# Kernel tuning notes

Hardware: AMD Instinct MI355X
Metric: run time of the kernel (lower is better)

Reference implementation:

```python
import jax, jax.numpy as jnp
import numpy as np

D = 1024
H = 16
HD = D // H
EPS = 1e-9


def setup_inputs() -> dict:
    key = jax.random.key(0)
    ks = jax.random.split(key, 16)
    B, Lq, Lk = 8, 512, 1024
    s = 0.02
    return {
        "q": jax.random.normal(ks[0], (B, Lq, D), jnp.float32),
        "q_mask": jnp.ones((B, Lq), jnp.bool_),
        "kv": jax.random.normal(ks[1], (B, Lk, D), jnp.float32),
        "kv_mask": jnp.ones((B, Lk), jnp.bool_),
        # MultiheadAttention packed in-proj + out-proj
        "in_proj_w": jax.random.normal(ks[2], (3 * D, D), jnp.float32) * s,
        "in_proj_b": jnp.zeros((3 * D,), jnp.float32),
        "out_w": jax.random.normal(ks[3], (D, D), jnp.float32) * s,
        "out_b": jnp.zeros((D,), jnp.float32),
        # shared LayerNorm
        "ln_g": jnp.ones((D,), jnp.float32),
        "ln_b": jnp.zeros((D,), jnp.float32),
        # FFN
        "w1": jax.random.normal(ks[4], (4 * D, D), jnp.float32) * s,
        "b1": jnp.zeros((4 * D,), jnp.float32),
        "w2": jax.random.normal(ks[5], (D, 4 * D), jnp.float32) * s,
        "b2": jnp.zeros((D,), jnp.float32),
        # gate MLP
        "gw1": jax.random.normal(ks[6], (D, 2 * D), jnp.float32) * s,
        "gb1": jnp.zeros((D,), jnp.float32),
        "gw2": jax.random.normal(ks[7], (1, D), jnp.float32) * s,
        "gb2": jnp.zeros((1,), jnp.float32),
    }


def _layer_norm(x, g, b, eps=1e-5):
    mu = x.mean(-1, keepdims=True)
    var = ((x - mu) ** 2).mean(-1, keepdims=True)
    return (x - mu) * jax.lax.rsqrt(var + eps) * g + b


def reference(q, q_mask, kv, kv_mask, in_proj_w, in_proj_b, out_w, out_b,
              ln_g, ln_b, w1, b1, w2, b2, gw1, gb1, gw2, gb2):
    B, Lq, _ = q.shape
    Lk = kv.shape[1]
    # packed projections (torch Linear convention: x @ W.T + b)
    qp = (q @ in_proj_w[:D].T + in_proj_b[:D]).reshape(B, Lq, H, HD)
    kp = (kv @ in_proj_w[D:2 * D].T + in_proj_b[D:2 * D]).reshape(B, Lk, H, HD)
    vp = (kv @ in_proj_w[2 * D:].T + in_proj_b[2 * D:]).reshape(B, Lk, H, HD)
    scores = jnp.einsum('bqhd,bkhd->bhqk', qp, kp) / np.sqrt(HD)  # (B,H,Lq,Lk)
    scores = jnp.where(kv_mask[:, None, None, :], scores, -1e30)
    attn = jax.nn.softmax(scores, axis=-1)
    ctx = jnp.einsum('bhqk,bkhd->bqhd', attn, vp).reshape(B, Lq, D)
    attn_out = ctx @ out_w.T + out_b
    # entropy over keys, normalized by log(Lk), averaged over heads
    p = jnp.clip(attn, EPS)
    ent = -(p * jnp.log(p)).sum(-1) / jnp.log(jnp.float32(Lk))  # (B,H,Lq)
    ent = ent.mean(axis=1)[..., None]  # (B,Lq,1)
    conf = jnp.clip(1.0 - ent, 0.0, 1.0)
    # gate MLP on [q, attn_out]
    h = jax.nn.gelu(jnp.concatenate([q, attn_out], -1) @ gw1.T + gb1, approximate=False)
    g = jax.nn.sigmoid(h @ gw2.T + gb2) * conf
    q2 = _layer_norm(q + attn_out * g, ln_g, ln_b)
    ffn = jax.nn.gelu(q2 @ w1.T + b1, approximate=False) @ w2.T + b2
    q2 = _layer_norm(q2 + ffn, ln_g, ln_b)
    return q2, ent
```

## Files before the change

kernel.cpp:

```cpp
#include <hip/hip_runtime.h>
#include <cstdint>
#include <cstddef>

typedef __bf16 bf16;
typedef __bf16 bf16x8 __attribute__((ext_vector_type(8)));
typedef __bf16 bf16x4 __attribute__((ext_vector_type(4)));
typedef float  f32x4  __attribute__((ext_vector_type(4)));

#define GLOAD_LDS16(g, l) __builtin_amdgcn_global_load_lds( \
    (const __attribute__((address_space(1))) unsigned int*)(g), \
    (__attribute__((address_space(3))) unsigned int*)(l), 16, 0, 0)

static constexpr int D_  = 1024;
static constexpr int H_  = 16;
static constexpr int HD_ = 64;
static constexpr int B_  = 8;
static constexpr int LQ_ = 512;
static constexpr int LK_ = 1024;
static constexpr int MQ_ = B_ * LQ_;
static constexpr float LOG2E_ = 1.4426950408889634f;
static constexpr float INV_LN_LK_ = 0.14426950408889634f;
static constexpr float CSHIFT_ = 8.0f;

__device__ __forceinline__ float gelu_f(float v) {
    return 0.5f * v * (1.0f + erff(v * 0.70710678118654752f));
}

__global__ __launch_bounds__(256)
void cast_all_k(const float* __restrict__ ipw, const float* __restrict__ outw,
                const float* __restrict__ w1,  const float* __restrict__ w2,
                const float* __restrict__ gw1, const float* __restrict__ q,
                const float* __restrict__ kv,
                bf16* __restrict__ ipw_b, bf16* __restrict__ outw_b,
                bf16* __restrict__ w1_b,  bf16* __restrict__ w2_b,
                bf16* __restrict__ gw1_b, bf16* __restrict__ x_b,
                bf16* __restrict__ kv_b) {
    const int b = blockIdx.x, t = threadIdx.x;
    const float* src; bf16* dst; long e;
    if (b < 1536)       { src = ipw;  dst = ipw_b;  e = (long)b * 2048; }
    else if (b < 2048)  { src = outw; dst = outw_b; e = (long)(b - 1536) * 2048; }
    else if (b < 4096)  { src = w1;   dst = w1_b;   e = (long)(b - 2048) * 2048; }
    else if (b < 6144)  { src = w2;   dst = w2_b;   e = (long)(b - 4096) * 2048; }
    else if (b < 7168)  { src = gw1;  dst = gw1_b;  e = (long)(b - 6144) * 2048; }
    else if (b < 11264) { src = kv;   dst = kv_b;   e = (long)(b - 7168) * 2048; }
    else {
        long e2 = (long)(b - 11264) * 2048 + t * 8;
        float4 a = *(const float4*)(q + e2);
        float4 c = *(const float4*)(q + e2 + 4);
        bf16x8 o;
        o[0]=(bf16)a.x; o[1]=(bf16)a.y; o[2]=(bf16)a.z; o[3]=(bf16)a.w;
        o[4]=(bf16)c.x; o[5]=(bf16)c.y; o[6]=(bf16)c.z; o[7]=(bf16)c.w;
        long row = e2 >> 10, col = e2 & 1023;
        *(bf16x8*)(x_b + row * 2048 + col) = o;
        return;
    }
    e += t * 8;
    float4 a = *(const float4*)(src + e);
    float4 c = *(const float4*)(src + e + 4);
    bf16x8 o;
    o[0]=(bf16)a.x; o[1]=(bf16)a.y; o[2]=(bf16)a.z; o[3]=(bf16)a.w;
    o[4]=(bf16)c.x; o[5]=(bf16)c.y; o[6]=(bf16)c.z; o[7]=(bf16)c.w;
    *(bf16x8*)(dst + e) = o;
}

template<int SPLITK>
__device__ __forceinline__
void gemmP_body(const bf16* __restrict__ A, int lda,
                const bf16* __restrict__ W, int ldw,
                const float* __restrict__ bias,
                bf16* __restrict__ Cb, int ldcb,
                float* __restrict__ Cf0, float* __restrict__ Cf1, int ldcf,
                int K, int aoff, int woff) {
    __shared__ __attribute__((aligned(16))) bf16 LDSp[3 * 8192];
    const int gx = gridDim.x, gy = gridDim.y;
    const int nwg = gx * gy * gridDim.z;
    const int flat = blockIdx.x + gx * (blockIdx.y + gy * blockIdx.z);
    const int swz = (flat & 7) * (nwg >> 3) + (flat >> 3);
    int rem = swz, z = 0;
    if (SPLITK) { z = swz / (gx * gy); rem = swz - z * (gx * gy); }
    const int by = rem / gx, bx = rem - by * gx;
    if (SPLITK) { A += (size_t)z * aoff; W += (size_t)z * woff; }
    float* Cf = (SPLITK && z) ? Cf1 : Cf0;

    const int t = threadIdx.x;
    const int w = t >> 6, l = t & 63, l15 = l & 15, lg = l >> 4;
    const int row0 = by * 128, col0 = bx * 128;
    const int wr = (w >> 1) * 64, wc = (w & 1) * 64;

    const int sr = t >> 2;
    const int sc = ((t & 3) ^ ((sr >> 1) & 3)) << 3;
    const bf16* pA0 = A + (size_t)(row0 + sr) * lda + sc;
    const bf16* pA1 = A + (size_t)(row0 + 64 + sr) * lda + sc;
    const bf16* pW0 = W + (size_t)(col0 + sr) * ldw + sc;
    const bf16* pW1 = W + (size_t)(col0 + 64 + sr) * ldw + sc;
    const int lo0 = w * 512, lo1 = 2048 + w * 512;

    auto STAGE = [&](int kt, int slot) {
        bf16* base = (bf16*)LDSp + slot * 8192;
        const int kc = kt * 32;
        GLOAD_LDS16(pA0 + kc, base + lo0);
        GLOAD_LDS16(pA1 + kc, base + lo1);
        GLOAD_LDS16(pW0 + kc, base + 4096 + lo0);
        GLOAD_LDS16(pW1 + kc, base + 4096 + lo1);
    };

    f32x4 acc[4][4];
#pragma unroll
    for (int m = 0; m < 4; ++m)
#pragma unroll
        for (int n = 0; n < 4; ++n) acc[m][n] = f32x4{0.f, 0.f, 0.f, 0.f};

    const int nk = K >> 5;
    STAGE(0, 0); STAGE(1, 1);
    asm volatile("s_waitcnt vmcnt(4)" ::: "memory");
    __builtin_amdgcn_s_barrier();

    int s0 = 0, s1 = 1, s2 = 2;
    const int kcol = (lg ^ ((l15 >> 1) & 3)) << 3;
    for (int kt = 0; kt < nk; ++kt) {
        const bf16* bufA = (const bf16*)LDSp + s0 * 8192;
        const bf16* bufB = bufA + 4096;
        bf16x8 af[4], bf4[4];
#pragma unroll
        for (int m = 0; m < 4; ++m)
            af[m] = *(const bf16x8*)&bufA[(wr + m * 16 + l15) * 32 + kcol];
#pragma unroll
        for (int n = 0; n < 4; ++n)
            bf4[n] = *(const bf16x8*)&bufB[(wc + n * 16 + l15) * 32 + kcol];
        if (kt + 2 < nk) STAGE(kt + 2, s2);
        __builtin_amdgcn_s_setprio(1);
#pragma unroll
        for (int m = 0; m < 4; ++m)
#pragma unroll
            for (int n = 0; n < 4; ++n)
                acc[m][n] = __builtin_amdgcn_mfma_f32_16x16x32_bf16(af[m], bf4[n], acc[m][n], 0, 0, 0);
        __builtin_amdgcn_s_setprio(0);
        asm volatile("s_waitcnt lgkmcnt(0)" ::: "memory");
        __builtin_amdgcn_sched_barrier(0);
        if (kt + 2 < nk) {
            asm volatile("s_waitcnt vmcnt(4)" ::: "memory");
        } else {
            asm volatile("s_waitcnt vmcnt(0)" ::: "memory");
        }
        __builtin_amdgcn_s_barrier();
        const int tmp = s0; s0 = s1; s1 = s2; s2 = tmp;
    }

    if (!SPLITK) {
        float bvn[4];
#pragma unroll
        for (int n = 0; n < 4; ++n) bvn[n] = bias[col0 + wc + n * 16 + l15];
        const int erow = l >> 2, ec = (l & 3) * 16;
#pragma unroll
        for (int m = 0; m < 4; ++m) {
            bf16* ep = (bf16*)LDSp + ((m & 1) * 4 + w) * 1152;
#pragma unroll
            for (int n = 0; n < 4; ++n)
#pragma unroll
                for (int r = 0; r < 4; ++r)
                    ep[(lg * 4 + r) * 72 + n * 16 + l15] = (bf16)(acc[m][n][r] + bvn[n]);
            asm volatile("s_waitcnt lgkmcnt(0)" ::: "memory");
            __builtin_amdgcn_sched_barrier(0);
            bf16x8 v8a = *(const bf16x8*)&ep[erow * 72 + ec];
            bf16x8 v8b = *(const bf16x8*)&ep[erow * 72 + ec + 8];
            const int grow = row0 + wr + m * 16 + erow;
            bf16* dst = Cb + (size_t)grow * ldcb + col0 + wc + ec;
            *(bf16x8*)dst = v8a;
            *(bf16x8*)(dst + 8) = v8b;
        }
    } else {
#pragma unroll
        for (int n = 0; n < 4; ++n) {
            int gcol = col0 + wc + n * 16 + l15;
#pragma unroll
            for (int m = 0; m < 4; ++m) {
                int grow = row0 + wr + m * 16 + lg * 4;
#pragma unroll
                for (int r = 0; r < 4; ++r)
                    Cf[(size_t)(grow + r) * ldcf + gcol] = acc[m][n][r];
            }
        }
    }
}

__global__ __launch_bounds__(256, 2)
void gemmP_qproj_k(const bf16* A, const bf16* W, const float* bias, bf16* Cb) {
    gemmP_body<0>(A, 2048, W, 1024, bias, Cb, 1024, nullptr, nullptr, 0, 1024, 0, 0);
}
__global__ __launch_bounds__(256, 2)
void gemmP_outproj_k(const bf16* A, const bf16* W, const float* bias, bf16* Cb) {
    gemmP_body<0>(A, 1024, W, 1024, bias, Cb, 2048, nullptr, nullptr, 0, 1024, 0, 0);
}
__global__ __launch_bounds__(256, 2)
void gemmP_gate2_k(const bf16* A, const bf16* W, float* C0, float* C1) {
    gemmP_body<1>(A, 2048, W, 2048, nullptr, nullptr, 0, C0, C1, 1024, 1024, 1024, 1024);
}
__global__ __launch_bounds__(256, 2)
void gemmP_ffn2_k(const bf16* A, const bf16* W, float* C0, float* C1) {
    gemmP_body<1>(A, 4096, W, 4096, nullptr, nullptr, 0, C0, C1, 1024, 2048, 2048, 2048);
}

template<int ACT>
__device__ __forceinline__
void gemm128x256_body(const bf16* __restrict__ A, int lda,
                      const bf16* __restrict__ W, int ldw,
                      const float* __restrict__ bias,
                      bf16* __restrict__ Cb, int ldcb, int K) {
    __shared__ __attribute__((aligned(16))) bf16 LDSb[2][12288];
    const int gx = gridDim.x;
    const int nwg = gx * gridDim.y;
    const int flat = blockIdx.x + gx * blockIdx.y;
    const int swz = (flat & 7) * (nwg >> 3) + (flat >> 3);
    const int by = swz / gx, bx = swz - by * gx;
    const int t = threadIdx.x;
    const int w = t >> 6, l = t & 63, l15 = l & 15, lg = l >> 4;
    const int wrr = w >> 2, wc = w & 3;
    const int row0 = by * 128, col0 = bx * 256;

    const int trow = t >> 2;
    const int scol = ((t & 3) ^ ((trow >> 1) & 3)) << 3;
    const bf16* pA  = A + (size_t)(row0 + trow) * lda + scol;
    const bf16* pB0 = W + (size_t)(col0 + trow) * ldw + scol;
    const bf16* pB1 = W + (size_t)(col0 + 128 + trow) * ldw + scol;
    const int ldsoA  = w * 512;
    const int ldsoB0 = 4096 + w * 512;
    const int ldsoB1 = 8192 + w * 512;

    f32x4 acc[4][4];
#pragma unroll
    for (int m = 0; m < 4; ++m)
#pragma unroll
        for (int n = 0; n < 4; ++n) acc[m][n] = f32x4{0.f, 0.f, 0.f, 0.f};

    const int nk = K >> 5;
    GLOAD_LDS16(pA,  (bf16*)LDSb[0] + ldsoA);
    GLOAD_LDS16(pB0, (bf16*)LDSb[0] + ldsoB0);
    GLOAD_LDS16(pB1, (bf16*)LDSb[0] + ldsoB1);

    for (int kt = 0; kt < nk; ++kt) {
        const int cur = kt & 1;
        if (kt + 1 < nk) {
            const int kc = (kt + 1) * 32;
            bf16* d = (bf16*)LDSb[cur ^ 1];
            GLOAD_LDS16(pA + kc,  d + ldsoA);
            GLOAD_LDS16(pB0 + kc, d + ldsoB0);
            GLOAD_LDS16(pB1 + kc, d + ldsoB1);
            asm volatile("s_waitcnt vmcnt(3)" ::: "memory");
        } else {
            asm volatile("s_waitcnt vmcnt(0)" ::: "memory");
        }
        __builtin_amdgcn_s_barrier();
        const bf16* bufA = (const bf16*)LDSb[cur];
        const bf16* bufB = bufA + 4096;
        const int kcol = (lg ^ ((l15 >> 1) & 3)) << 3;
        bf16x8 bf4[4];
#pragma unroll
        for (int n = 0; n < 4; ++n)
            bf4[n] = *(const bf16x8*)&bufB[(wc * 64 + n * 16 + l15) * 32 + kcol];
#pragma unroll
        for (int m = 0; m < 4; ++m) {
            bf16x8 afm = *(const bf16x8*)&bufA[(wrr * 64 + m * 16 + l15) * 32 + kcol];
#pragma unroll
            for (int n = 0; n < 4; ++n)
                acc[m][n] = __builtin_amdgcn_mfma_f32_16x16x32_bf16(afm, bf4[n], acc[m][n], 0, 0, 0);
        }
        asm volatile("s_waitcnt lgkmcnt(0)" ::: "memory");
        __builtin_amdgcn_sched_barrier(0);
        __builtin_amdgcn_s_barrier();
    }

    float bvn[4];
#pragma unroll
    for (int n = 0; n < 4; ++n) bvn[n] = bias[col0 + wc * 64 + n * 16 + l15];
    const int erow = l >> 2, ec = (l & 3) * 16;
#pragma unroll
    for (int m = 0; m < 4; ++m) {
        bf16* ep = (bf16*)LDSb + ((m & 1) * 8 + w) * 1152;
#pragma unroll
        for (int n = 0; n < 4; ++n)
#pragma unroll
            for (int r = 0; r < 4; ++r) {
                float v = acc[m][n][r] + bvn[n];
                if (ACT) v = gelu_f(v);
                ep[(lg * 4 + r) * 72 + n * 16 + l15] = (bf16)v;
            }
        asm volatile("s_waitcnt lgkmcnt(0)" ::: "memory");
        __builtin_amdgcn_sched_barrier(0);
        bf16x8 v8a = *(const bf16x8*)&ep[erow * 72 + ec];
        bf16x8 v8b = *(const bf16x8*)&ep[erow * 72 + ec + 8];
        const int grow = row0 + wrr * 64 + m * 16 + erow;
        bf16* dst = Cb + (size_t)grow * ldcb + col0 + wc * 64 + ec;
        *(bf16x8*)dst = v8a;
        *(bf16x8*)(dst + 8) = v8b;
    }
}

__global__ __launch_bounds__(512, 4)
void gemmA_kvproj_k(const bf16* A, const bf16* W, const float* bias, bf16* Cb) {
    gemm128x256_body<0>(A, 1024, W, 1024, bias, Cb, 2048, 1024);
}
__global__ __launch_bounds__(512, 4)
void gemmA_ffn1_k(const bf16* A, const bf16* W, const float* bias, bf16* Cb) {
    gemm128x256_body<1>(A, 1024, W, 1024, bias, Cb, 4096, 1024);
}

__device__ __forceinline__ float red16sum(float v) {
    v += __shfl_xor(v, 1, 64);
    v += __shfl_xor(v, 2, 64);
    v += __shfl_xor(v, 4, 64);
    v += __shfl_xor(v, 8, 64);
    return v;
}

__global__ __launch_bounds__(256)
void attn_k(const bf16* __restrict__ Qp, const bf16* __restrict__ KVp,
            bf16* __restrict__ ctx, float* __restrict__ entm) {
    __shared__ __attribute__((aligned(16))) bf16 Ks[64 * 72];
    __shared__ __attribute__((aligned(16))) bf16 Vts[64 * 72];
    __shared__ __attribute__((aligned(16))) bf16 Ps[4][16 * 72];
    const int t = threadIdx.x, w = t >> 6, l = t & 63;
    const int l15 = l & 15, lg = l >> 4;
    const int h = blockIdx.x, b = blockIdx.y, qt = blockIdx.z;
    const int qrow0 = b * LQ_ + qt * 64 + w * 16;

    bf16x8 aq[2];
#pragma unroll
    for (int kk = 0; kk < 2; ++kk)
        aq[kk] = *(const bf16x8*)(Qp + (size_t)(qrow0 + l15) * D_ + h * HD_ + kk * 32 + lg * 8);

    f32x4 o[4];
    float Zp[4], S1p[4];
#pragma unroll
    for (int n = 0; n < 4; ++n) o[n] = f32x4{0.f, 0.f, 0.f, 0.f};
#pragma unroll
    for (int r = 0; r < 4; ++r) { Zp[r] = 0.f; S1p[r] = 0.f; }

    const float K1 = 0.125f * LOG2E_;
    const float K0 = -CSHIFT_ * LOG2E_;

    for (int c = 0; c < LK_ / 64; ++c) {
        __syncthreads();
        const int kbase = b * LK_ + c * 64;
#pragma unroll
        for (int i = 0; i < 2; ++i) {
            int f = i * 256 + t;
            int key = f >> 3, seg = f & 7;
            const bf16* kvrow = KVp + (size_t)(kbase + key) * 2048 + h * HD_ + seg * 8;
            bf16x8 k8 = *(const bf16x8*)kvrow;
            bf16x8 v8 = *(const bf16x8*)(kvrow + 1024);
            *(bf16x8*)&Ks[key * 72 + seg * 8] = k8;
            int vcol = key ^ (seg << 3);
#pragma unroll
            for (int j = 0; j < 8; ++j) Vts[(seg * 8 + j) * 72 + vcol] = v8[j];
        }
        __syncthreads();

        f32x4 s[4];
#pragma unroll
        for (int n = 0; n < 4; ++n) {
            s[n] = f32x4{0.f, 0.f, 0.f, 0.f};
#pragma unroll
            for (int kk = 0; kk < 2; ++kk) {
                bf16x8 bk = *(const bf16x8*)&Ks[(n * 16 + l15) * 72 + kk * 32 + lg * 8];
                s[n] = __builtin_amdgcn_mfma_f32_16x16x32_bf16(aq[kk], bk, s[n], 0, 0, 0);
            }
        }

        float p[4][4];
#pragma unroll
        for (int r = 0; r < 4; ++r) {
#pragma unroll
            for (int n = 0; n < 4; ++n) {
                float sv = s[n][r];
                float pv = exp2f(fmaf(sv, K1, K0));
                p[n][r] = pv;
                Zp[r] += pv;
                S1p[r] = fmaf(pv, sv, S1p[r]);
            }
        }

#pragma unroll
        for (int r = 0; r < 4; ++r)
#pragma unroll
            for (int n = 0; n < 4; ++n)
                Ps[w][(lg * 4 + r) * 72 + ((n ^ lg) << 4) + l15] = (bf16)p[n][r];

        bf16x8 ap[2];
#pragma unroll
        for (int kk = 0; kk < 2; ++kk)
            ap[kk] = *(const bf16x8*)&Ps[w][l15 * 72 + ((kk * 32 + lg * 8) ^ (((l15 >> 2) & 3) << 4))];
#pragma unroll
        for (int n = 0; n < 4; ++n) {
            const int segd = (n * 2 + (l15 >> 3)) & 7;
#pragma unroll
            for (int kk = 0; kk < 2; ++kk) {
                bf16x8 bv = *(const bf16x8*)&Vts[(n * 16 + l15) * 72 + (((kk * 4 + lg) ^ segd) << 3)];
                o[n] = __builtin_amdgcn_mfma_f32_16x16x32_bf16(ap[kk], bv, o[n], 0, 0, 0);
            }
        }
    }

#pragma unroll
    for (int r = 0; r < 4; ++r) {
        float Zr = red16sum(Zp[r]);
        float S1r = red16sum(S1p[r]) * 0.125f;
        float inv = 1.0f / Zr;
        int grow = qrow0 + lg * 4 + r;
#pragma unroll
        for (int n = 0; n < 4; ++n)
            ctx[(size_t)grow * D_ + h * HD_ + n * 16 + l15] = (bf16)(o[n][r] * inv);
        if (l15 == 0) {
            float ent = (CSHIFT_ + logf(Zr) - S1r * inv) * INV_LN_LK_ * (1.0f / 16.0f);
            atomicAdd(&entm[grow], ent);
        }
    }
}

__device__ __forceinline__ float blk_sum(float v, float* sb) {
#pragma unroll
    for (int m = 1; m < 64; m <<= 1) v += __shfl_xor(v, m, 64);
    int w = threadIdx.x >> 6;
    __syncthreads();
    if ((threadIdx.x & 63) == 0) sb[w] = v;
    __syncthreads();
    return sb[0] + sb[1] + sb[2] + sb[3];
}
__device__ __forceinline__ float2 blk_sum2(float2 v, float* sb) {
#pragma unroll
    for (int m = 1; m < 64; m <<= 1) {
        v.x += __shfl_xor(v.x, m, 64);
        v.y += __shfl_xor(v.y, m, 64);
    }
    int w = threadIdx.x >> 6;
    __syncthreads();
    if ((threadIdx.x & 63) == 0) { sb[w * 2] = v.x; sb[w * 2 + 1] = v.y; }
    __syncthreads();
    return make_float2(sb[0] + sb[2] + sb[4] + sb[6], sb[1] + sb[3] + sb[5] + sb[7]);
}

__global__ __launch_bounds__(256)
void gate_ln1_k(const float* __restrict__ qin, const bf16* __restrict__ xb,
                const float* __restrict__ gp0, const float* __restrict__ gp1,
                const float* __restrict__ gb1, const float* __restrict__ gw2,
                const float* __restrict__ gb2, const float* __restrict__ entm,
                const float* __restrict__ lng, const float* __restrict__ lnb,
                float* __restrict__ q2f, bf16* __restrict__ q2b) {
    __shared__ float sb[8];
    const int row = blockIdx.x, t = threadIdx.x, c0 = t * 4;
    float4 p0 = *(const float4*)(gp0 + (size_t)row * D_ + c0);
    float4 p1 = *(const float4*)(gp1 + (size_t)row * D_ + c0);
    float4 hb = *(const float4*)(gb1 + c0);
    float h0 = gelu_f(p0.x + p1.x + hb.x);
    float h1 = gelu_f(p0.y + p1.y + hb.y);
    float h2 = gelu_f(p0.z + p1.z + hb.z);
    float h3 = gelu_f(p0.w + p1.w + hb.w);
    float4 g4 = *(const float4*)(gw2 + c0);
    float dot = h0 * g4.x + h1 * g4.y + h2 * g4.z + h3 * g4.w;
    dot = blk_sum(dot, sb);
    float g = 1.0f / (1.0f + expf(-(dot + gb2[0])));
    float conf = fminf(fmaxf(1.0f - entm[row], 0.0f), 1.0f);
    g *= conf;
    float4 qv = *(const float4*)(qin + (size_t)row * D_ + c0);
    bf16x4 a4 = *(const bf16x4*)(xb + (size_t)row * 2048 + 1024 + c0);
    float y[4] = { qv.x + (float)a4[0] * g, qv.y + (float)a4[1] * g,
                   qv.z + (float)a4[2] * g, qv.w + (float)a4[3] * g };
    float2 ss = blk_sum2(make_float2(y[0] + y[1] + y[2] + y[3],
                                     y[0]*y[0] + y[1]*y[1] + y[2]*y[2] + y[3]*y[3]), sb);
    float mu = ss.x * (1.0f / D_);
    float var = ss.y * (1.0f / D_) - mu * mu;
    float rs = rsqrtf(var + 1e-5f);
    float4 gg = *(const float4*)(lng + c0);
    float4 bb = *(const float4*)(lnb + c0);
    float o0 = (y[0] - mu) * rs * gg.x + bb.x;
    float o1 = (y[1] - mu) * rs * gg.y + bb.y;
    float o2 = (y[2] - mu) * rs * gg.z + bb.z;
    float o3 = (y[3] - mu) * rs * gg.w + bb.w;
    *(float4*)(q2f + (size_t)row * D_ + c0) = make_float4(o0, o1, o2, o3);
    bf16x4 ob; ob[0] = (bf16)o0; ob[1] = (bf16)o1; ob[2] = (bf16)o2; ob[3] = (bf16)o3;
    *(bf16x4*)(q2b + (size_t)row * D_ + c0) = ob;
}

__global__ __launch_bounds__(256)
void ln2_k(const float* __restrict__ q2f, const float* __restrict__ fp0,
           const float* __restrict__ fp1, const float* __restrict__ b2,
           const float* __restrict__ lng, const float* __restrict__ lnb,
           float* __restrict__ outp) {
    __shared__ float sb[8];
    const int row = blockIdx.x, t = threadIdx.x, c0 = t * 4;
    float4 a = *(const float4*)(q2f + (size_t)row * D_ + c0);
    float4 f0 = *(const float4*)(fp0 + (size_t)row * D_ + c0);
    float4 f1 = *(const float4*)(fp1 + (size_t)row * D_ + c0);
    float4 bv = *(const float4*)(b2 + c0);
    float y[4] = { a.x + f0.x + f1.x + bv.x, a.y + f0.y + f1.y + bv.y,
                   a.z + f0.z + f1.z + bv.z, a.w + f0.w + f1.w + bv.w };
    float2 ss = blk_sum2(make_float2(y[0] + y[1] + y[2] + y[3],
                                     y[0]*y[0] + y[1]*y[1] + y[2]*y[2] + y[3]*y[3]), sb);
    float mu = ss.x * (1.0f / D_);
    float var = ss.y * (1.0f / D_) - mu * mu;
    float rs = rsqrtf(var + 1e-5f);
    float4 gg = *(const float4*)(lng + c0);
    float4 bb = *(const float4*)(lnb + c0);
    *(float4*)(outp + (size_t)row * D_ + c0) = make_float4(
        (y[0] - mu) * rs * gg.x + bb.x, (y[1] - mu) * rs * gg.y + bb.y,
        (y[2] - mu) * rs * gg.z + bb.z, (y[3] - mu) * rs * gg.w + bb.w);
}

extern "C" void kernel_launch(void* const* d_in, const int* in_sizes, int n_in,
                              void* d_out, int out_size, void* d_ws, size_t ws_size,
                              hipStream_t stream) {
    (void)in_sizes; (void)n_in; (void)out_size; (void)ws_size;
    const float* q    = (const float*)d_in[0];
    const float* kv   = (const float*)d_in[2];
    const float* ipw  = (const float*)d_in[4];
    const float* ipb  = (const float*)d_in[5];
    const float* outw = (const float*)d_in[6];
    const float* outb = (const float*)d_in[7];
    const float* lng  = (const float*)d_in[8];
    const float* lnb  = (const float*)d_in[9];
    const float* w1   = (const float*)d_in[10];
    const float* b1   = (const float*)d_in[11];
    const float* w2   = (const float*)d_in[12];
    const float* b2   = (const float*)d_in[13];
    const float* gw1  = (const float*)d_in[14];
    const float* gb1  = (const float*)d_in[15];
    const float* gw2  = (const float*)d_in[16];
    const float* gb2  = (const float*)d_in[17];

    char* ws = (char*)d_ws;
    const size_t MB = 1u << 20;
    bf16*  ipw_b  = (bf16*)(ws + 0);
    bf16*  outw_b = (bf16*)(ws + 6 * MB);
    bf16*  w1_b   = (bf16*)(ws + 8 * MB);
    bf16*  w2_b   = (bf16*)(ws + 16 * MB);
    bf16*  gw1_b  = (bf16*)(ws + 24 * MB);
    bf16*  x_b    = (bf16*)(ws + 28 * MB);
    bf16*  kv_b   = (bf16*)(ws + 44 * MB);
    bf16*  Qp     = (bf16*)(ws + 60 * MB);
    bf16*  KVp    = (bf16*)(ws + 68 * MB);
    bf16*  ctx    = (bf16*)(ws + 100 * MB);
    float* gp0    = (float*)(ws + 44 * MB);
    float* gp1    = (float*)(ws + 60 * MB);
    float* q2f    = (float*)(ws + 76 * MB);
    bf16*  q2b    = (bf16*)(ws + 100 * MB);
    bf16*  h1     = (bf16*)(ws + 44 * MB);
    float* fp0    = (float*)(ws + 28 * MB);
    float* fp1    = (float*)(ws + 0);

    float* out  = (float*)d_out;
    float* entm = out + (size_t)MQ_ * D_;

    (void)hipMemsetAsync(entm, 0, (size_t)MQ_ * sizeof(float), stream);

    cast_all_k<<<13312, 256, 0, stream>>>(ipw, outw, w1, w2, gw1, q, kv,
                                          ipw_b, outw_b, w1_b, w2_b, gw1_b, x_b, kv_b);

    gemmP_qproj_k<<<dim3(8, 32), 256, 0, stream>>>(x_b, ipw_b, ipb, Qp);
    gemmA_kvproj_k<<<dim3(8, 64), 512, 0, stream>>>(kv_b, ipw_b + 1024 * 1024, ipb + 1024, KVp);
    attn_k<<<dim3(H_, B_, LQ_ / 64), 256, 0, stream>>>(Qp, KVp, ctx, entm);
    gemmP_outproj_k<<<dim3(8, 32), 256, 0, stream>>>(ctx, outw_b, outb, x_b + 1024);
    gemmP_gate2_k<<<dim3(8, 32, 2), 256, 0, stream>>>(x_b, gw1_b, gp0, gp1);
    gate_ln1_k<<<MQ_, 256, 0, stream>>>(q, x_b, gp0, gp1, gb1, gw2, gb2, entm, lng, lnb, q2f, q2b);
    gemmA_ffn1_k<<<dim3(16, 32), 512, 0, stream>>>(q2b, w1_b, b1, h1);
    gemmP_ffn2_k<<<dim3(8, 32, 2), 256, 0, stream>>>(h1, w2_b, fp0, fp1);
    ln2_k<<<MQ_, 256, 0, stream>>>(q2f, fp0, fp1, b2, lng, lnb, out);
}
```

Before: 295.1 us.

## Produce transposed V from projection GEMM and double-buffer K/V via direct LDS loads

Splits the fused KV projection into a K projection and a V projection computed as W_v·kv^T, so V is written already transposed (head-dim major) with a per-row bias. The attention kernel then stages K and V tiles with global_load_lds into double-buffered, XOR-swizzled LDS and prefetches the next chunk while computing the current one. This removes the scalar in-LDS transpose of V and the register round-trip through LDS. In exchange there is an extra GEMM launch, and the transposed-output GEMM writes long rows with a strided layout.

```diff
diff --git a/kernel.cpp b/kernel.cpp
--- a/kernel.cpp
+++ b/kernel.cpp
@@ -18,6 +18,7 @@
 static constexpr int LQ_ = 512;
 static constexpr int LK_ = 1024;
 static constexpr int MQ_ = B_ * LQ_;
+static constexpr int MK_ = B_ * LK_;
 static constexpr float LOG2E_ = 1.4426950408889634f;
 static constexpr float INV_LN_LK_ = 0.14426950408889634f;
 static constexpr float CSHIFT_ = 8.0f;
@@ -200,7 +201,7 @@
     gemmP_body<1>(A, 4096, W, 4096, nullptr, nullptr, 0, C0, C1, 1024, 2048, 2048, 2048);
 }
 
-template<int ACT>
+template<int ACT, int ROWBIAS>
 __device__ __forceinline__
 void gemm128x256_body(const bf16* __restrict__ A, int lda,
                       const bf16* __restrict__ W, int ldw,
@@ -269,18 +270,26 @@
         __builtin_amdgcn_s_barrier();
     }
 
+    const int erow = l >> 2, ec = (l & 3) * 16;
     float bvn[4];
-#pragma unroll
-    for (int n = 0; n < 4; ++n) bvn[n] = bias[col0 + wc * 64 + n * 16 + l15];
-    const int erow = l >> 2, ec = (l & 3) * 16;
+    if (!ROWBIAS) {
+#pragma unroll
+        for (int n = 0; n < 4; ++n) bvn[n] = bias[col0 + wc * 64 + n * 16 + l15];
+    }
 #pragma unroll
     for (int m = 0; m < 4; ++m) {
+        float bvr[4];
+        if (ROWBIAS) {
+#pragma unroll
+            for (int r = 0; r < 4; ++r)
+                bvr[r] = bias[row0 + wrr * 64 + m * 16 + lg * 4 + r];
+        }
         bf16* ep = (bf16*)LDSb + ((m & 1) * 8 + w) * 1152;
 #pragma unroll
         for (int n = 0; n < 4; ++n)
 #pragma unroll
             for (int r = 0; r < 4; ++r) {
-                float v = acc[m][n][r] + bvn[n];
+                float v = acc[m][n][r] + (ROWBIAS ? bvr[r] : bvn[n]);
                 if (ACT) v = gelu_f(v);
                 ep[(lg * 4 + r) * 72 + n * 16 + l15] = (bf16)v;
             }
@@ -296,12 +305,16 @@
 }
 
 __global__ __launch_bounds__(512, 4)
-void gemmA_kvproj_k(const bf16* A, const bf16* W, const float* bias, bf16* Cb) {
-    gemm128x256_body<0>(A, 1024, W, 1024, bias, Cb, 2048, 1024);
+void gemmA_kproj_k(const bf16* A, const bf16* W, const float* bias, bf16* Cb) {
+    gemm128x256_body<0, 0>(A, 1024, W, 1024, bias, Cb, 1024, 1024);
+}
+__global__ __launch_bounds__(512, 4)
+void gemmA_vprojT_k(const bf16* A, const bf16* W, const float* bias, bf16* Cb) {
+    gemm128x256_body<0, 1>(A, 1024, W, 1024, bias, Cb, 8192, 1024);
 }
 __global__ __launch_bounds__(512, 4)
 void gemmA_ffn1_k(const bf16* A, const bf16* W, const float* bias, bf16* Cb) {
-    gemm128x256_body<1>(A, 1024, W, 1024, bias, Cb, 4096, 1024);
+    gemm128x256_body<1, 0>(A, 1024, W, 1024, bias, Cb, 4096, 1024);
 }
 
 __device__ __forceinline__ float red16sum(float v) {
@@ -313,10 +326,11 @@
 }
 
 __global__ __launch_bounds__(256)
-void attn_k(const bf16* __restrict__ Qp, const bf16* __restrict__ KVp,
-            bf16* __restrict__ ctx, float* __restrict__ entm) {
-    __shared__ __attribute__((aligned(16))) bf16 Ks[64 * 72];
-    __shared__ __attribute__((aligned(16))) bf16 Vts[64 * 72];
+void attn_k(const bf16* __restrict__ Qp, const bf16* __restrict__ Kp,
+            const bf16* __restrict__ Vt, bf16* __restrict__ ctx,
+            float* __restrict__ entm) {
+    __shared__ __attribute__((aligned(16))) bf16 Ks[2][64 * 64];
+    __shared__ __attribute__((aligned(16))) bf16 Vs[2][64 * 64];
     __shared__ __attribute__((aligned(16))) bf16 Ps[4][16 * 72];
     const int t = threadIdx.x, w = t >> 6, l = t & 63;
     const int l15 = l & 15, lg = l >> 4;
@@ -328,6 +342,22 @@
     for (int kk = 0; kk < 2; ++kk)
         aq[kk] = *(const bf16x8*)(Qp + (size_t)(qrow0 + l15) * D_ + h * HD_ + kk * 32 + lg * 8);
 
+    const int r0 = t >> 3, r1 = 32 + (t >> 3), j = t & 7;
+    const bf16* pK0 = Kp + (size_t)(b * LK_ + r0) * 1024 + h * HD_ + ((j ^ (r0 & 7)) << 3);
+    const bf16* pK1 = Kp + (size_t)(b * LK_ + r1) * 1024 + h * HD_ + ((j ^ (r1 & 7)) << 3);
+    const bf16* pV0 = Vt + (size_t)(h * HD_ + r0) * (size_t)MK_ + b * LK_ + ((j ^ (r0 & 7)) << 3);
+    const bf16* pV1 = Vt + (size_t)(h * HD_ + r1) * (size_t)MK_ + b * LK_ + ((j ^ (r1 & 7)) << 3);
+    const int ldsoL = w * 512, ldsoH = 2048 + w * 512;
+
+    auto STAGE = [&](int c, int buf) {
+        const size_t kadv = (size_t)c * 64 * 1024;
+        const size_t vadv = (size_t)c * 64;
+        GLOAD_LDS16(pK0 + kadv, (bf16*)Ks[buf] + ldsoL);
+        GLOAD_LDS16(pK1 + kadv, (bf16*)Ks[buf] + ldsoH);
+        GLOAD_LDS16(pV0 + vadv, (bf16*)Vs[buf] + ldsoL);
+        GLOAD_LDS16(pV1 + vadv, (bf16*)Vs[buf] + ldsoH);
+    };
+
     f32x4 o[4];
     float Zp[4], S1p[4];
 #pragma unroll
@@ -337,23 +367,15 @@
 
     const float K1 = 0.125f * LOG2E_;
     const float K0 = -CSHIFT_ * LOG2E_;
+    const int swk = l15 & 7;
+
+    STAGE(0, 0);
+    asm volatile("s_waitcnt vmcnt(0)" ::: "memory");
+    __builtin_amdgcn_s_barrier();
 
     for (int c = 0; c < LK_ / 64; ++c) {
-        __syncthreads();
-        const int kbase = b * LK_ + c * 64;
-#pragma unroll
-        for (int i = 0; i < 2; ++i) {
-            int f = i * 256 + t;
-            int key = f >> 3, seg = f & 7;
-            const bf16* kvrow = KVp + (size_t)(kbase + key) * 2048 + h * HD_ + seg * 8;
-            bf16x8 k8 = *(const bf16x8*)kvrow;
-            bf16x8 v8 = *(const bf16x8*)(kvrow + 1024);
-            *(bf16x8*)&Ks[key * 72 + seg * 8] = k8;
-            int vcol = key ^ (seg << 3);
-#pragma unroll
-            for (int j = 0; j < 8; ++j) Vts[(seg * 8 + j) * 72 + vcol] = v8[j];
-        }
-        __syncthreads();
+        const int buf = c & 1;
+        if (c + 1 < LK_ / 64) STAGE(c + 1, buf ^ 1);
 
         f32x4 s[4];
 #pragma unroll
@@ -361,7 +383,7 @@
             s[n] = f32x4{0.f, 0.f, 0.f, 0.f};
 #pragma unroll
             for (int kk = 0; kk < 2; ++kk) {
-                bf16x8 bk = *(const bf16x8*)&Ks[(n * 16 + l15) * 72 + kk * 32 + lg * 8];
+                bf16x8 bk = *(const bf16x8*)&Ks[buf][(n * 16 + l15) * 64 + ((((kk << 2) | lg) ^ swk) << 3)];
                 s[n] = __builtin_amdgcn_mfma_f32_16x16x32_bf16(aq[kk], bk, s[n], 0, 0, 0);
             }
         }
@@ -390,14 +412,17 @@
         for (int kk = 0; kk < 2; ++kk)
             ap[kk] = *(const bf16x8*)&Ps[w][l15 * 72 + ((kk * 32 + lg * 8) ^ (((l15 >> 2) & 3) << 4))];
 #pragma unroll
-        for (int n = 0; n < 4; ++n) {
-            const int segd = (n * 2 + (l15 >> 3)) & 7;
+        for (int n = 0; n < 4; ++n)
 #pragma unroll
             for (int kk = 0; kk < 2; ++kk) {
-                bf16x8 bv = *(const bf16x8*)&Vts[(n * 16 + l15) * 72 + (((kk * 4 + lg) ^ segd) << 3)];
+                bf16x8 bv = *(const bf16x8*)&Vs[buf][(n * 16 + l15) * 64 + ((((kk << 2) | lg) ^ swk) << 3)];
                 o[n] = __builtin_amdgcn_mfma_f32_16x16x32_bf16(ap[kk], bv, o[n], 0, 0, 0);
             }
-        }
+
+        asm volatile("s_waitcnt lgkmcnt(0)" ::: "memory");
+        __builtin_amdgcn_sched_barrier(0);
+        asm volatile("s_waitcnt vmcnt(0)" ::: "memory");
+        __builtin_amdgcn_s_barrier();
     }
 
 #pragma unroll
@@ -536,7 +561,8 @@
     bf16*  x_b    = (bf16*)(ws + 28 * MB);
     bf16*  kv_b   = (bf16*)(ws + 44 * MB);
     bf16*  Qp     = (bf16*)(ws + 60 * MB);
-    bf16*  KVp    = (bf16*)(ws + 68 * MB);
+    bf16*  Kp     = (bf16*)(ws + 68 * MB);
+    bf16*  Vt     = (bf16*)(ws + 84 * MB);
     bf16*  ctx    = (bf16*)(ws + 100 * MB);
     float* gp0    = (float*)(ws + 44 * MB);
     float* gp1    = (float*)(ws + 60 * MB);
@@ -555,8 +581,9 @@
                                           ipw_b, outw_b, w1_b, w2_b, gw1_b, x_b, kv_b);
 
     gemmP_qproj_k<<<dim3(8, 32), 256, 0, stream>>>(x_b, ipw_b, ipb, Qp);
-    gemmA_kvproj_k<<<dim3(8, 64), 512, 0, stream>>>(kv_b, ipw_b + 1024 * 1024, ipb + 1024, KVp);
-    attn_k<<<dim3(H_, B_, LQ_ / 64), 256, 0, stream>>>(Qp, KVp, ctx, entm);
+    gemmA_kproj_k<<<dim3(4, 64), 512, 0, stream>>>(kv_b, ipw_b + 1024 * 1024, ipb + 1024, Kp);
+    gemmA_vprojT_k<<<dim3(32, 8), 512, 0, stream>>>(ipw_b + 2048 * 1024, kv_b, ipb + 2048, Vt);
+    attn_k<<<dim3(H_, B_, LQ_ / 64), 256, 0, stream>>>(Qp, Kp, Vt, ctx, entm);
     gemmP_outproj_k<<<dim3(8, 32), 256, 0, stream>>>(ctx, outw_b, outb, x_b + 1024);
     gemmP_gate2_k<<<dim3(8, 32, 2), 256, 0, stream>>>(x_b, gw1_b, gp0, gp1);
     gate_ln1_k<<<MQ_, 256, 0, stream>>>(q, x_b, gp0, gp1, gb1, gw2, gb2, entm, lng, lnb, q2f, q2b);
```

Result: slower. 316.6 us (+7.3%).
